# Kernel tuning notes

Hardware: AMD Instinct MI355X
Metric: run time of the kernel (lower is better)

The kernel has to match this reference:

```python
import jax, jax.numpy as jnp
import numpy as np

N, NQ, M, DQ, DK, DV, H = 4, 512, 512, 256, 256, 256, 256


def setup_inputs() -> dict:
    key = jax.random.key(0)
    ks = jax.random.split(key, 6)
    scale_q = 1.0 / np.sqrt(DQ)
    scale_k = 1.0 / np.sqrt(DK)
    scale_v = 1.0 / np.sqrt(H)
    return {
        "query": jax.random.normal(ks[0], (N, NQ, DQ), jnp.float32),
        "key": jax.random.normal(ks[1], (N, M, DK), jnp.float32),
        "value": jax.random.normal(ks[2], (N, M, DV), jnp.float32),
        "W_q": jax.random.normal(ks[3], (DQ, H), jnp.float32) * scale_q,
        "W_k": jax.random.normal(ks[4], (DK, H), jnp.float32) * scale_k,
        "W_v": jax.random.normal(ks[5], (H,), jnp.float32) * scale_v,
    }


def reference(query, key, value, W_q, W_k, W_v):
    # project: (N, n, H) and (N, m, H)
    q = jnp.einsum("bnd,dh->bnh", query, W_q)
    k = jnp.einsum("bmd,dh->bmh", key, W_k)
    # broadcast add -> (N, n, m, H), tanh, project H->1 -> scores (N, n, m)
    scores = jnp.einsum("bnmh,h->bnm", jnp.tanh(q[:, :, None, :] + k[:, None, :, :]), W_v)
    attn = jax.nn.softmax(scores, axis=-1)  # (N, n, m)
    return jnp.einsum("bnm,bmv->bnv", attn, value)
```

## Files before the change

### kernel.cpp

```cpp
#include <hip/hip_runtime.h>
#include <hip/hip_bf16.h>

#define NB 4
#define NQL 512
#define ML 512
#define DDIM 256
#define HDIM 256
#define PSZ ((size_t)NB * NQL * ML)

static constexpr float TWO_LOG2E = 2.8853900817779268f;
static constexpr float LOG2E     = 1.4426950408889634f;

__global__ __launch_bounds__(256) void proj_kernel(
    const float* __restrict__ q_src, const float* __restrict__ k_src,
    const float* __restrict__ Wq,    const float* __restrict__ Wk,
    float* __restrict__ EqT,         float* __restrict__ EkT)
{
    const int z = blockIdx.z;
    const int b = z & 3;
    const int which = z >> 2;
    const float* __restrict__ src  = which ? k_src : q_src;
    const float* __restrict__ W    = which ? Wk    : Wq;
    float* __restrict__       outT = which ? EkT   : EqT;

    const int l0 = blockIdx.x * 32;
    const int h0 = blockIdx.y * 64;
    const int t  = threadIdx.x;
    const int tx = t & 15;
    const int ty = t >> 4;

    __shared__ __align__(16) float sX[32][36];
    __shared__ __align__(16) float sW[32][68];

    float acc[2][4];
    #pragma unroll
    for (int i = 0; i < 2; i++)
        #pragma unroll
        for (int j = 0; j < 4; j++) acc[i][j] = 0.f;

    const int llA = t >> 3, dgA = t & 7;
    const int ddB = t >> 3, hgB = t & 7;

    for (int d0 = 0; d0 < DDIM; d0 += 32) {
        float4 xv = *(const float4*)&src[(size_t)(b * NQL + l0 + llA) * DDIM + d0 + dgA * 4];
        const float* wrow = &W[(size_t)(d0 + ddB) * HDIM + h0 + hgB * 8];
        float4 wa = ((const float4*)wrow)[0];
        float4 wb = ((const float4*)wrow)[1];
        __syncthreads();
        sX[dgA * 4 + 0][llA] = xv.x;
        sX[dgA * 4 + 1][llA] = xv.y;
        sX[dgA * 4 + 2][llA] = xv.z;
        sX[dgA * 4 + 3][llA] = xv.w;
        *(float4*)&sW[ddB][hgB * 8]     = wa;
        *(float4*)&sW[ddB][hgB * 8 + 4] = wb;
        __syncthreads();
        #pragma unroll
        for (int dd = 0; dd < 32; dd++) {
            float4 w4 = *(const float4*)&sW[dd][tx * 4];
            float2 x2 = *(const float2*)&sX[dd][ty * 2];
            acc[0][0] = fmaf(x2.x, w4.x, acc[0][0]);
            acc[0][1] = fmaf(x2.x, w4.y, acc[0][1]);
            acc[0][2] = fmaf(x2.x, w4.z, acc[0][2]);
            acc[0][3] = fmaf(x2.x, w4.w, acc[0][3]);
            acc[1][0] = fmaf(x2.y, w4.x, acc[1][0]);
            acc[1][1] = fmaf(x2.y, w4.y, acc[1][1]);
            acc[1][2] = fmaf(x2.y, w4.z, acc[1][2]);
            acc[1][3] = fmaf(x2.y, w4.w, acc[1][3]);
        }
    }

    #pragma unroll
    for (int j = 0; j < 4; j++) {
        float2 o;
        o.x = __builtin_amdgcn_exp2f(acc[0][j] * TWO_LOG2E);
        o.y = __builtin_amdgcn_exp2f(acc[1][j] * TWO_LOG2E);
        *(float2*)&outT[(size_t)(b * HDIM + h0 + tx * 4 + j) * NQL + l0 + ty * 2] = o;
    }
}

__global__ __launch_bounds__(256) void scores_kernel(
    const float* __restrict__ EqT, const float* __restrict__ EkT,
    const float* __restrict__ Wv, float* __restrict__ Sp)
{
    const int z  = blockIdx.z;
    const int b  = z & 3;
    const int p  = z >> 2;
    const int h0 = p * 64;
    const int m0 = blockIdx.x * 64;
    const int n0 = blockIdx.y * 64;
    const int t  = threadIdx.x;
    const int tx = t & 15;
    const int ty = t >> 4;

    __shared__ __align__(16) float sQ[64][68];
    __shared__ __align__(16) float sK[64][68];
    __shared__ __align__(16) float sWV[64];

    {
        const int hh = t >> 2, cg = t & 3;
        const float* qsrc = &EqT[(size_t)(b * HDIM + h0 + hh) * NQL + n0 + cg * 16];
        const float* ksrc = &EkT[(size_t)(b * HDIM + h0 + hh) * ML  + m0 + cg * 16];
        float4 q0 = ((const float4*)qsrc)[0];
        float4 q1 = ((const float4*)qsrc)[1];
        float4 q2 = ((const float4*)qsrc)[2];
        float4 q3 = ((const float4*)qsrc)[3];
        float4 k0 = ((const float4*)ksrc)[0];
        float4 k1 = ((const float4*)ksrc)[1];
        float4 k2 = ((const float4*)ksrc)[2];
        float4 k3 = ((const float4*)ksrc)[3];
        *(float4*)&sQ[hh][cg * 16 + 0]  = q0;
        *(float4*)&sQ[hh][cg * 16 + 4]  = q1;
        *(float4*)&sQ[hh][cg * 16 + 8]  = q2;
        *(float4*)&sQ[hh][cg * 16 + 12] = q3;
        *(float4*)&sK[hh][cg * 16 + 0]  = k0;
        *(float4*)&sK[hh][cg * 16 + 4]  = k1;
        *(float4*)&sK[hh][cg * 16 + 8]  = k2;
        *(float4*)&sK[hh][cg * 16 + 12] = k3;
        if (t < 64) sWV[t] = Wv[h0 + t];
    }
    __syncthreads();

    float acc[4][4];
    #pragma unroll
    for (int i = 0; i < 4; i++)
        #pragma unroll
        for (int j = 0; j < 4; j++) acc[i][j] = 0.f;
    float swv = 0.f;

    for (int h4 = 0; h4 < 16; h4++) {
        float4 wv4 = *(const float4*)&sWV[h4 * 4];
        float wvs[4] = {wv4.x, wv4.y, wv4.z, wv4.w};
        #pragma unroll
        for (int u = 0; u < 4; u++) {
            const int hh = h4 * 4 + u;
            float4 q4 = *(const float4*)&sQ[hh][ty * 4];
            float4 k4 = *(const float4*)&sK[hh][tx * 4];
            const float wv  = wvs[u];
            swv += wv;
            const float nw2 = -2.0f * wv;
            float qs[4] = {q4.x, q4.y, q4.z, q4.w};
            #pragma unroll
            for (int i = 0; i < 4; i++) {
                float a0 = fmaf(qs[i], k4.x, 1.0f);
                float a1 = fmaf(qs[i], k4.y, 1.0f);
                float a2 = fmaf(qs[i], k4.z, 1.0f);
                float a3 = fmaf(qs[i], k4.w, 1.0f);
                float r01 = __builtin_amdgcn_rcpf(a0 * a1);
                float r23 = __builtin_amdgcn_rcpf(a2 * a3);
                acc[i][0] = fmaf(nw2, r01 * a1, acc[i][0]);
                acc[i][1] = fmaf(nw2, r01 * a0, acc[i][1]);
                acc[i][2] = fmaf(nw2, r23 * a3, acc[i][2]);
                acc[i][3] = fmaf(nw2, r23 * a2, acc[i][3]);
            }
        }
    }

    float* srow = &Sp[p * PSZ + (size_t)(b * NQL + n0 + ty * 4) * ML + m0 + tx * 4];
    #pragma unroll
    for (int i = 0; i < 4; i++) {
        float4 o = {swv + acc[i][0], swv + acc[i][1],
                    swv + acc[i][2], swv + acc[i][3]};
        *(float4*)&srow[(size_t)i * ML] = o;
    }
}

__global__ __launch_bounds__(256) void sav_kernel(
    const float* __restrict__ Sp, const float* __restrict__ V,
    float* __restrict__ O)
{
    const int b  = blockIdx.z;
    const int v0 = blockIdx.x * 64;
    const int n0 = blockIdx.y * 16;
    const int t  = threadIdx.x;

    __shared__ __align__(16) float sP[16][516];
    __shared__ __align__(16) float sRed[16][16];

    const int row = t >> 4;
    const int seg = t & 15;
    {
        const float* srow = &Sp[(size_t)(b * NQL + n0 + row) * ML + seg * 32];
        float psum = 0.f;
        #pragma unroll
        for (int i = 0; i < 8; i++) {
            float4 s0 = ((const float4*)(srow + 0 * PSZ))[i];
            float4 s1 = ((const float4*)(srow + 1 * PSZ))[i];
            float4 s2 = ((const float4*)(srow + 2 * PSZ))[i];
            float4 s3 = ((const float4*)(srow + 3 * PSZ))[i];
            float4 sv;
            sv.x = (s0.x + s1.x) + (s2.x + s3.x);
            sv.y = (s0.y + s1.y) + (s2.y + s3.y);
            sv.z = (s0.z + s1.z) + (s2.z + s3.z);
            sv.w = (s0.w + s1.w) + (s2.w + s3.w);
            float4 e;
            e.x = __builtin_amdgcn_exp2f(sv.x * LOG2E);
            e.y = __builtin_amdgcn_exp2f(sv.y * LOG2E);
            e.z = __builtin_amdgcn_exp2f(sv.z * LOG2E);
            e.w = __builtin_amdgcn_exp2f(sv.w * LOG2E);
            *(float4*)&sP[row][seg * 32 + i * 4] = e;
            psum += (e.x + e.y) + (e.z + e.w);
        }
        sRed[row][seg] = psum;
    }
    __syncthreads();

    const int tx = t & 15;
    const int ty = t >> 4;
    float rs = 0.f;
    #pragma unroll
    for (int i = 0; i < 16; i++) rs += sRed[tx][i];
    const float inv = 1.0f / rs;

    float4 acc = {0.f, 0.f, 0.f, 0.f};
    const float* vbase = &V[(size_t)b * ML * DDIM + v0 + ty * 4];
    #pragma unroll 2
    for (int m4 = 0; m4 < 128; m4++) {
        float4 a4 = *(const float4*)&sP[tx][m4 * 4];
        float4 va = *(const float4*)&vbase[(size_t)(m4 * 4 + 0) * DDIM];
        float4 vb = *(const float4*)&vbase[(size_t)(m4 * 4 + 1) * DDIM];
        float4 vc = *(const float4*)&vbase[(size_t)(m4 * 4 + 2) * DDIM];
        float4 vd = *(const float4*)&vbase[(size_t)(m4 * 4 + 3) * DDIM];
        acc.x = fmaf(a4.x, va.x, acc.x);
        acc.y = fmaf(a4.x, va.y, acc.y);
        acc.z = fmaf(a4.x, va.z, acc.z);
        acc.w = fmaf(a4.x, va.w, acc.w);
        acc.x = fmaf(a4.y, vb.x, acc.x);
        acc.y = fmaf(a4.y, vb.y, acc.y);
        acc.z = fmaf(a4.y, vb.z, acc.z);
        acc.w = fmaf(a4.y, vb.w, acc.w);
        acc.x = fmaf(a4.z, vc.x, acc.x);
        acc.y = fmaf(a4.z, vc.y, acc.y);
        acc.z = fmaf(a4.z, vc.z, acc.z);
        acc.w = fmaf(a4.z, vc.w, acc.w);
        acc.x = fmaf(a4.w, vd.x, acc.x);
        acc.y = fmaf(a4.w, vd.y, acc.y);
        acc.z = fmaf(a4.w, vd.z, acc.z);
        acc.w = fmaf(a4.w, vd.w, acc.w);
    }

    float4 o;
    o.x = acc.x * inv; o.y = acc.y * inv; o.z = acc.z * inv; o.w = acc.w * inv;
    *(float4*)&O[(size_t)(b * NQL + n0 + tx) * DDIM + v0 + ty * 4] = o;
}

extern "C" void kernel_launch(void* const* d_in, const int* in_sizes, int n_in,
                              void* d_out, int out_size, void* d_ws, size_t ws_size,
                              hipStream_t stream)
{
    const float* query = (const float*)d_in[0];
    const float* key   = (const float*)d_in[1];
    const float* value = (const float*)d_in[2];
    const float* Wq    = (const float*)d_in[3];
    const float* Wk    = (const float*)d_in[4];
    const float* Wv    = (const float*)d_in[5];
    float* out = (float*)d_out;

    float* EqT = (float*)d_ws;
    float* EkT = EqT + (size_t)NB * HDIM * NQL;
    float* Sp  = EkT + (size_t)NB * HDIM * ML;

    dim3 gProj(NQL / 32, HDIM / 64, NB * 2);
    proj_kernel<<<gProj, 256, 0, stream>>>(query, key, Wq, Wk, EqT, EkT);

    dim3 gSc(ML / 64, NQL / 64, NB * 4);
    scores_kernel<<<gSc, 256, 0, stream>>>(EqT, EkT, Wv, Sp);

    dim3 gSav(DDIM / 64, NQL / 16, NB);
    sav_kernel<<<gSav, 256, 0, stream>>>(Sp, value, out);
}
```

Measured before the change: 157.8 us.

## Drop H-split partial scores; loop all H chunks per block with prefetch

The scores kernel no longer splits the hidden dimension across four blocks that each write partial score planes. Each block now loops over all four 64-wide H chunks, register-prefetching the next chunk's Q/K tiles while computing the current one, and applies the exp before writing a single probability plane. This removes three extra score planes of global writes and the four-way read-and-sum plus exp in the softmax/AV kernel, which now just loads P and does coalesced row loads. The trade-off is four times fewer blocks in the scores kernel (256 instead of 1024), so occupancy and parallelism are lower, plus extra barriers per chunk; the AV loop unroll also rises from 2 to 4.

```diff
diff --git a/kernel.cpp b/kernel.cpp
--- a/kernel.cpp
+++ b/kernel.cpp
@@ -6,7 +6,6 @@
 #define ML 512
 #define DDIM 256
 #define HDIM 256
-#define PSZ ((size_t)NB * NQL * ML)
 
 static constexpr float TWO_LOG2E = 2.8853900817779268f;
 static constexpr float LOG2E     = 1.4426950408889634f;
@@ -80,45 +79,30 @@
 
 __global__ __launch_bounds__(256) void scores_kernel(
     const float* __restrict__ EqT, const float* __restrict__ EkT,
-    const float* __restrict__ Wv, float* __restrict__ Sp)
-{
-    const int z  = blockIdx.z;
-    const int b  = z & 3;
-    const int p  = z >> 2;
-    const int h0 = p * 64;
+    const float* __restrict__ Wv, float* __restrict__ P)
+{
+    const int b  = blockIdx.z;
     const int m0 = blockIdx.x * 64;
     const int n0 = blockIdx.y * 64;
     const int t  = threadIdx.x;
     const int tx = t & 15;
     const int ty = t >> 4;
 
-    __shared__ __align__(16) float sQ[64][68];
-    __shared__ __align__(16) float sK[64][68];
-    __shared__ __align__(16) float sWV[64];
-
-    {
-        const int hh = t >> 2, cg = t & 3;
-        const float* qsrc = &EqT[(size_t)(b * HDIM + h0 + hh) * NQL + n0 + cg * 16];
-        const float* ksrc = &EkT[(size_t)(b * HDIM + h0 + hh) * ML  + m0 + cg * 16];
-        float4 q0 = ((const float4*)qsrc)[0];
-        float4 q1 = ((const float4*)qsrc)[1];
-        float4 q2 = ((const float4*)qsrc)[2];
-        float4 q3 = ((const float4*)qsrc)[3];
-        float4 k0 = ((const float4*)ksrc)[0];
-        float4 k1 = ((const float4*)ksrc)[1];
-        float4 k2 = ((const float4*)ksrc)[2];
-        float4 k3 = ((const float4*)ksrc)[3];
-        *(float4*)&sQ[hh][cg * 16 + 0]  = q0;
-        *(float4*)&sQ[hh][cg * 16 + 4]  = q1;
-        *(float4*)&sQ[hh][cg * 16 + 8]  = q2;
-        *(float4*)&sQ[hh][cg * 16 + 12] = q3;
-        *(float4*)&sK[hh][cg * 16 + 0]  = k0;
-        *(float4*)&sK[hh][cg * 16 + 4]  = k1;
-        *(float4*)&sK[hh][cg * 16 + 8]  = k2;
-        *(float4*)&sK[hh][cg * 16 + 12] = k3;
-        if (t < 64) sWV[t] = Wv[h0 + t];
-    }
-    __syncthreads();
+    __shared__ __align__(16) float sQ[64][64];
+    __shared__ __align__(16) float sK[64][64];
+    __shared__ __align__(16) float sWV[256];
+
+    const int hhA = t >> 2, cgA = t & 3;
+    const float* qsrc = &EqT[(size_t)(b * HDIM + hhA) * NQL + n0 + cgA * 16];
+    const float* ksrc = &EkT[(size_t)(b * HDIM + hhA) * ML  + m0 + cgA * 16];
+
+    float4 pq[4], pk[4];
+    #pragma unroll
+    for (int i = 0; i < 4; i++) {
+        pq[i] = ((const float4*)qsrc)[i];
+        pk[i] = ((const float4*)ksrc)[i];
+    }
+    sWV[t] = Wv[t];
 
     float acc[4][4];
     #pragma unroll
@@ -127,45 +111,67 @@
         for (int j = 0; j < 4; j++) acc[i][j] = 0.f;
     float swv = 0.f;
 
-    for (int h4 = 0; h4 < 16; h4++) {
-        float4 wv4 = *(const float4*)&sWV[h4 * 4];
-        float wvs[4] = {wv4.x, wv4.y, wv4.z, wv4.w};
-        #pragma unroll
-        for (int u = 0; u < 4; u++) {
-            const int hh = h4 * 4 + u;
-            float4 q4 = *(const float4*)&sQ[hh][ty * 4];
-            float4 k4 = *(const float4*)&sK[hh][tx * 4];
-            const float wv  = wvs[u];
-            swv += wv;
-            const float nw2 = -2.0f * wv;
-            float qs[4] = {q4.x, q4.y, q4.z, q4.w};
+    for (int c = 0; c < 4; c++) {
+        if (c > 0) __syncthreads();
+        #pragma unroll
+        for (int i = 0; i < 4; i++) {
+            *(float4*)&sQ[hhA][cgA * 16 + i * 4] = pq[i];
+            *(float4*)&sK[hhA][cgA * 16 + i * 4] = pk[i];
+        }
+        __syncthreads();
+        if (c < 3) {
+            const float* qn = qsrc + (size_t)(c + 1) * 64 * NQL;
+            const float* kn = ksrc + (size_t)(c + 1) * 64 * ML;
             #pragma unroll
             for (int i = 0; i < 4; i++) {
-                float a0 = fmaf(qs[i], k4.x, 1.0f);
-                float a1 = fmaf(qs[i], k4.y, 1.0f);
-                float a2 = fmaf(qs[i], k4.z, 1.0f);
-                float a3 = fmaf(qs[i], k4.w, 1.0f);
-                float r01 = __builtin_amdgcn_rcpf(a0 * a1);
-                float r23 = __builtin_amdgcn_rcpf(a2 * a3);
-                acc[i][0] = fmaf(nw2, r01 * a1, acc[i][0]);
-                acc[i][1] = fmaf(nw2, r01 * a0, acc[i][1]);
-                acc[i][2] = fmaf(nw2, r23 * a3, acc[i][2]);
-                acc[i][3] = fmaf(nw2, r23 * a2, acc[i][3]);
+                pq[i] = ((const float4*)qn)[i];
+                pk[i] = ((const float4*)kn)[i];
             }
         }
-    }
-
-    float* srow = &Sp[p * PSZ + (size_t)(b * NQL + n0 + ty * 4) * ML + m0 + tx * 4];
+        #pragma unroll 4
+        for (int h4 = 0; h4 < 16; h4++) {
+            float4 wv4 = *(const float4*)&sWV[c * 64 + h4 * 4];
+            float wvs[4] = {wv4.x, wv4.y, wv4.z, wv4.w};
+            #pragma unroll
+            for (int u = 0; u < 4; u++) {
+                const int hh = h4 * 4 + u;
+                float4 q4 = *(const float4*)&sQ[hh][ty * 4];
+                float4 k4 = *(const float4*)&sK[hh][tx * 4];
+                const float wv  = wvs[u];
+                swv += wv;
+                const float nw2 = -2.0f * wv;
+                float qs[4] = {q4.x, q4.y, q4.z, q4.w};
+                #pragma unroll
+                for (int i = 0; i < 4; i++) {
+                    float a0 = fmaf(qs[i], k4.x, 1.0f);
+                    float a1 = fmaf(qs[i], k4.y, 1.0f);
+                    float a2 = fmaf(qs[i], k4.z, 1.0f);
+                    float a3 = fmaf(qs[i], k4.w, 1.0f);
+                    float r01 = __builtin_amdgcn_rcpf(a0 * a1);
+                    float r23 = __builtin_amdgcn_rcpf(a2 * a3);
+                    acc[i][0] = fmaf(nw2, r01 * a1, acc[i][0]);
+                    acc[i][1] = fmaf(nw2, r01 * a0, acc[i][1]);
+                    acc[i][2] = fmaf(nw2, r23 * a3, acc[i][2]);
+                    acc[i][3] = fmaf(nw2, r23 * a2, acc[i][3]);
+                }
+            }
+        }
+    }
+
+    float* prow = &P[(size_t)(b * NQL + n0 + ty * 4) * ML + m0 + tx * 4];
     #pragma unroll
     for (int i = 0; i < 4; i++) {
-        float4 o = {swv + acc[i][0], swv + acc[i][1],
-                    swv + acc[i][2], swv + acc[i][3]};
-        *(float4*)&srow[(size_t)i * ML] = o;
+        float4 o;
+        o.x = __builtin_amdgcn_exp2f((swv + acc[i][0]) * LOG2E);
+        o.y = __builtin_amdgcn_exp2f((swv + acc[i][1]) * LOG2E);
+        o.z = __builtin_amdgcn_exp2f((swv + acc[i][2]) * LOG2E);
+        o.w = __builtin_amdgcn_exp2f((swv + acc[i][3]) * LOG2E);
+        *(float4*)&prow[(size_t)i * ML] = o;
     }
 }
 
 __global__ __launch_bounds__(256) void sav_kernel(
-    const float* __restrict__ Sp, const float* __restrict__ V,
+    const float* __restrict__ P, const float* __restrict__ V,
     float* __restrict__ O)
 {
     const int b  = blockIdx.z;
@@ -176,36 +182,23 @@
     __shared__ __align__(16) float sP[16][516];
     __shared__ __align__(16) float sRed[16][16];
 
-    const int row = t >> 4;
-    const int seg = t & 15;
     {
-        const float* srow = &Sp[(size_t)(b * NQL + n0 + row) * ML + seg * 32];
+        const int row = t >> 4;
+        const int l16 = t & 15;
+        const float4* prow = (const float4*)&P[(size_t)(b * NQL + n0 + row) * ML];
         float psum = 0.f;
         #pragma unroll
         for (int i = 0; i < 8; i++) {
-            float4 s0 = ((const float4*)(srow + 0 * PSZ))[i];
-            float4 s1 = ((const float4*)(srow + 1 * PSZ))[i];
-            float4 s2 = ((const float4*)(srow + 2 * PSZ))[i];
-            float4 s3 = ((const float4*)(srow + 3 * PSZ))[i];
-            float4 sv;
-            sv.x = (s0.x + s1.x) + (s2.x + s3.x);
-            sv.y = (s0.y + s1.y) + (s2.y + s3.y);
-            sv.z = (s0.z + s1.z) + (s2.z + s3.z);
-            sv.w = (s0.w + s1.w) + (s2.w + s3.w);
-            float4 e;
-            e.x = __builtin_amdgcn_exp2f(sv.x * LOG2E);
-            e.y = __builtin_amdgcn_exp2f(sv.y * LOG2E);
-            e.z = __builtin_amdgcn_exp2f(sv.z * LOG2E);
-            e.w = __builtin_amdgcn_exp2f(sv.w * LOG2E);
-            *(float4*)&sP[row][seg * 32 + i * 4] = e;
+            float4 e = prow[l16 + 16 * i];
+            *(float4*)&sP[row][(l16 + 16 * i) * 4] = e;
             psum += (e.x + e.y) + (e.z + e.w);
         }
-        sRed[row][seg] = psum;
+        sRed[row][l16] = psum;
     }
     __syncthreads();
 
-    const int tx = t & 15;
-    const int ty = t >> 4;
+    const int tx = t >> 4;
+    const int ty = t & 15;
     float rs = 0.f;
     #pragma unroll
     for (int i = 0; i < 16; i++) rs += sRed[tx][i];
@@ -213,7 +206,7 @@
 
     float4 acc = {0.f, 0.f, 0.f, 0.f};
     const float* vbase = &V[(size_t)b * ML * DDIM + v0 + ty * 4];
-    #pragma unroll 2
+    #pragma unroll 4
     for (int m4 = 0; m4 < 128; m4++) {
         float4 a4 = *(const float4*)&sP[tx][m4 * 4];
         float4 va = *(const float4*)&vbase[(size_t)(m4 * 4 + 0) * DDIM];
@@ -257,14 +250,14 @@
 
     float* EqT = (float*)d_ws;
     float* EkT = EqT + (size_t)NB * HDIM * NQL;
-    float* Sp  = EkT + (size_t)NB * HDIM * ML;
+    float* P   = EkT + (size_t)NB * HDIM * ML;
 
     dim3 gProj(NQL / 32, HDIM / 64, NB * 2);
     proj_kernel<<<gProj, 256, 0, stream>>>(query, key, Wq, Wk, EqT, EkT);
 
-    dim3 gSc(ML / 64, NQL / 64, NB * 4);
-    scores_kernel<<<gSc, 256, 0, stream>>>(EqT, EkT, Wv, Sp);
+    dim3 gSc(ML / 64, NQL / 64, NB);
+    scores_kernel<<<gSc, 256, 0, stream>>>(EqT, EkT, Wv, P);
 
     dim3 gSav(DDIM / 64, NQL / 16, NB);
-    sav_kernel<<<gSav, 256, 0, stream>>>(Sp, value, out);
-}
+    sav_kernel<<<gSav, 256, 0, stream>>>(P, value, out);
+}
```

Measured after the change: 156.8 us. Within noise of the previous version (-0.7%).

## Split partial-score reduction and exp into separate kernel before SAV

Applied to the files above, without the earlier changes.

Adds a reduce kernel that sums the four partial score slabs and applies exp once per element, writing a single probability matrix. The SAV kernel then reads that matrix with coalesced float4 loads instead of reducing four slabs itself. Previously each of the four v-column blocks recomputed the reduction and exp redundantly. The thread mapping in SAV is swapped so consecutive threads cover adjacent V columns, and the unroll of the V loop is raised. The cost is an extra kernel launch plus an extra write and read of the full score matrix, and more workspace.

```diff
diff --git a/kernel.cpp b/kernel.cpp
--- a/kernel.cpp
+++ b/kernel.cpp
@@ -164,8 +164,24 @@
     }
 }
 
+__global__ __launch_bounds__(256) void reduce_kernel(
+    const float* __restrict__ Sp, float* __restrict__ P)
+{
+    const size_t row_off = (size_t)blockIdx.x * ML;
+    const int t = threadIdx.x;
+    const float2* s0 = (const float2*)&Sp[row_off + 0 * PSZ];
+    const float2* s1 = (const float2*)&Sp[row_off + 1 * PSZ];
+    const float2* s2 = (const float2*)&Sp[row_off + 2 * PSZ];
+    const float2* s3 = (const float2*)&Sp[row_off + 3 * PSZ];
+    float2 a = s0[t], b = s1[t], c = s2[t], d = s3[t];
+    float2 o;
+    o.x = __builtin_amdgcn_exp2f(((a.x + b.x) + (c.x + d.x)) * LOG2E);
+    o.y = __builtin_amdgcn_exp2f(((a.y + b.y) + (c.y + d.y)) * LOG2E);
+    ((float2*)&P[row_off])[t] = o;
+}
+
 __global__ __launch_bounds__(256) void sav_kernel(
-    const float* __restrict__ Sp, const float* __restrict__ V,
+    const float* __restrict__ P, const float* __restrict__ V,
     float* __restrict__ O)
 {
     const int b  = blockIdx.z;
@@ -176,36 +192,23 @@
     __shared__ __align__(16) float sP[16][516];
     __shared__ __align__(16) float sRed[16][16];
 
-    const int row = t >> 4;
-    const int seg = t & 15;
     {
-        const float* srow = &Sp[(size_t)(b * NQL + n0 + row) * ML + seg * 32];
+        const int row = t >> 4;
+        const int l16 = t & 15;
+        const float4* prow = (const float4*)&P[(size_t)(b * NQL + n0 + row) * ML];
         float psum = 0.f;
         #pragma unroll
         for (int i = 0; i < 8; i++) {
-            float4 s0 = ((const float4*)(srow + 0 * PSZ))[i];
-            float4 s1 = ((const float4*)(srow + 1 * PSZ))[i];
-            float4 s2 = ((const float4*)(srow + 2 * PSZ))[i];
-            float4 s3 = ((const float4*)(srow + 3 * PSZ))[i];
-            float4 sv;
-            sv.x = (s0.x + s1.x) + (s2.x + s3.x);
-            sv.y = (s0.y + s1.y) + (s2.y + s3.y);
-            sv.z = (s0.z + s1.z) + (s2.z + s3.z);
-            sv.w = (s0.w + s1.w) + (s2.w + s3.w);
-            float4 e;
-            e.x = __builtin_amdgcn_exp2f(sv.x * LOG2E);
-            e.y = __builtin_amdgcn_exp2f(sv.y * LOG2E);
-            e.z = __builtin_amdgcn_exp2f(sv.z * LOG2E);
-            e.w = __builtin_amdgcn_exp2f(sv.w * LOG2E);
-            *(float4*)&sP[row][seg * 32 + i * 4] = e;
+            float4 e = prow[l16 + 16 * i];
+            *(float4*)&sP[row][(l16 + 16 * i) * 4] = e;
             psum += (e.x + e.y) + (e.z + e.w);
         }
-        sRed[row][seg] = psum;
+        sRed[row][l16] = psum;
     }
     __syncthreads();
 
-    const int tx = t & 15;
-    const int ty = t >> 4;
+    const int tx = t >> 4;
+    const int ty = t & 15;
     float rs = 0.f;
     #pragma unroll
     for (int i = 0; i < 16; i++) rs += sRed[tx][i];
@@ -213,7 +216,7 @@
 
     float4 acc = {0.f, 0.f, 0.f, 0.f};
     const float* vbase = &V[(size_t)b * ML * DDIM + v0 + ty * 4];
-    #pragma unroll 2
+    #pragma unroll 4
     for (int m4 = 0; m4 < 128; m4++) {
         float4 a4 = *(const float4*)&sP[tx][m4 * 4];
         float4 va = *(const float4*)&vbase[(size_t)(m4 * 4 + 0) * DDIM];
@@ -258,6 +261,7 @@
     float* EqT = (float*)d_ws;
     float* EkT = EqT + (size_t)NB * HDIM * NQL;
     float* Sp  = EkT + (size_t)NB * HDIM * ML;
+    float* P   = Sp  + 4 * PSZ;
 
     dim3 gProj(NQL / 32, HDIM / 64, NB * 2);
     proj_kernel<<<gProj, 256, 0, stream>>>(query, key, Wq, Wk, EqT, EkT);
@@ -265,6 +269,8 @@
     dim3 gSc(ML / 64, NQL / 64, NB * 4);
     scores_kernel<<<gSc, 256, 0, stream>>>(EqT, EkT, Wv, Sp);
 
+    reduce_kernel<<<dim3(NB * NQL), 256, 0, stream>>>(Sp, P);
+
     dim3 gSav(DDIM / 64, NQL / 16, NB);
-    sav_kernel<<<gSav, 256, 0, stream>>>(Sp, value, out);
-}
+    sav_kernel<<<gSav, 256, 0, stream>>>(P, value, out);
+}
```

Result: faster. 144.8 us (-8.2%).
